# Performance work log

Hardware: AMD Instinct MI355X
Metric: run time of the kernel (lower is better)

Reference implementation:

```python
import jax, jax.numpy as jnp
import numpy as np

CTX_SIZE = 4096
LAYER = 1
N_EMBD = 1024
HEAD_SIZE = 64
B, T = 4, 4096


def setup_inputs() -> dict:
    key = jax.random.key(0)
    ks = jax.random.split(key, 4)
    s = 1.0 / np.sqrt(N_EMBD)
    return {
        "x": jax.random.normal(ks[0], (B, T, N_EMBD), dtype=jnp.float32),
        "Wq": jax.random.normal(ks[1], (N_EMBD, HEAD_SIZE), dtype=jnp.float32) * s,
        "bq": jnp.zeros((HEAD_SIZE,), dtype=jnp.float32),
        "Wk": jax.random.normal(ks[2], (N_EMBD, HEAD_SIZE), dtype=jnp.float32) * s,
        "bk": jnp.zeros((HEAD_SIZE,), dtype=jnp.float32),
        "Wv": jax.random.normal(ks[3], (N_EMBD, HEAD_SIZE), dtype=jnp.float32) * s,
        "bv": jnp.zeros((HEAD_SIZE,), dtype=jnp.float32),
    }


def reference(x, Wq, bq, Wk, bk, Wv, bv):
    Bx, Tx, C = x.shape
    t = CTX_SIZE // (2 ** LAYER)
    cut = min(Tx, t)  # static: shapes are concrete under jit

    k = x @ Wk + bk                      # [B, T, H]
    q = x[:, -cut:, :] @ Wq + bq         # [B, cut, H] (fade: queries on last cut tokens)
    v = x @ Wv + bv                      # [B, T, H]

    att = jnp.einsum("bqh,bkh->bqk", q, k) * (C ** -0.5)  # [B, cut, T]

    # row i corresponds to absolute query position (T - cut + i); causal: key j <= that pos
    q_pos = jnp.arange(cut) + (Tx - cut)   # [cut]
    k_pos = jnp.arange(Tx)                 # [T]
    mask = k_pos[None, :] <= q_pos[:, None]  # [cut, T], True = keep
    att = jnp.where(mask[None, :, :], att, -jnp.inf)
    att = jax.nn.softmax(att, axis=-1)
    # dropout p=0.0 (eval mode): identity

    out = jnp.einsum("bqk,bkh->bqh", att, v)  # [B, cut, H]
    return out
```

## Files before the change

### kernel.cpp

```cpp
#include <hip/hip_runtime.h>

#define BB 4
#define TT 4096
#define CUT 2048
#define CE 1024
#define HD 64
#define QSC 0.045084220027780106f

typedef unsigned short u16;
typedef unsigned int u32;
typedef __attribute__((ext_vector_type(8))) short bf16x8;
typedef __attribute__((ext_vector_type(4))) float f32x4;

__device__ __forceinline__ u16 f2b(float f) {
  union { float f; unsigned u; } v; v.f = f;
  unsigned r = v.u + 0x7fffu + ((v.u >> 16) & 1u);
  return (u16)(r >> 16);
}

__device__ __forceinline__ u32 cvtpk(float lo, float hi) {
  u32 r;
  asm("v_cvt_pk_bf16_f32 %0, %1, %2" : "=v"(r) : "v"(lo), "v"(hi));
  return r;
}

__global__ void wtrans_k(const float* __restrict__ Wk, const float* __restrict__ Wv,
                         const float* __restrict__ Wq, u16* __restrict__ w3f) {
  int id = blockIdx.x * 256 + threadIdx.x;
  int j    = id & 7;
  int lane = (id >> 3) & 63;
  int f    = id >> 9;
  int kstep = f & 31;
  int mnt   = f >> 5;
  int m  = mnt >> 2;
  int nt = mnt & 3;
  int k   = kstep * 32 + (lane >> 4) * 8 + j;
  int col = nt * 16 + (lane & 15);
  const float* W = (m == 0) ? Wk : (m == 1) ? Wv : Wq;
  w3f[id] = f2b(W[k * 64 + col]);
}

__launch_bounds__(256, 2)
__global__ void proj_k(const float* __restrict__ x, const u16* __restrict__ w3f,
                       const float* __restrict__ bk, const float* __restrict__ bv,
                       const float* __restrict__ bq,
                       u16* __restrict__ Kb, u16* __restrict__ Vb, u16* __restrict__ Qb) {
  __shared__ f32x4 cl[2][2][12][64];
  const int tid  = threadIdx.x;
  const int lane = tid & 63;
  const int kh   = tid >> 6;
  const int l15  = lane & 15;
  const int g    = lane >> 4;
  const int r0   = blockIdx.x * 32;

  f32x4 acc[2][12];
  #pragma unroll
  for (int h = 0; h < 2; ++h)
    #pragma unroll
    for (int t = 0; t < 12; ++t) acc[h][t] = (f32x4){0.f, 0.f, 0.f, 0.f};

  const float* x0 = x + (size_t)(r0 + l15) * CE;
  const float* x1 = x + (size_t)(r0 + 16 + l15) * CE;

  #pragma unroll
  for (int kc = 0; kc < 8; ++kc) {
    const int ko = kh * 256 + kc * 32 + g * 8;
    bf16x8 a0, a1;
    {
      f32x4 xa = *(const f32x4*)(x0 + ko);
      f32x4 xb = *(const f32x4*)(x0 + ko + 4);
      f32x4 ya = *(const f32x4*)(x1 + ko);
      f32x4 yb = *(const f32x4*)(x1 + ko + 4);
      #pragma unroll
      for (int j = 0; j < 4; ++j) {
        a0[j] = (short)f2b(xa[j]); a0[j + 4] = (short)f2b(xb[j]);
        a1[j] = (short)f2b(ya[j]); a1[j + 4] = (short)f2b(yb[j]);
      }
    }
    const int kstep = kh * 8 + kc;
    #pragma unroll
    for (int mnt = 0; mnt < 12; ++mnt) {
      bf16x8 bfr = *(const bf16x8*)&w3f[(size_t)(mnt * 32 + kstep) * 512 + lane * 8];
      acc[0][mnt] = __builtin_amdgcn_mfma_f32_16x16x32_bf16(a0, bfr, acc[0][mnt], 0, 0, 0);
      acc[1][mnt] = __builtin_amdgcn_mfma_f32_16x16x32_bf16(a1, bfr, acc[1][mnt], 0, 0, 0);
    }
  }

  if (kh >= 2) {
    #pragma unroll
    for (int h = 0; h < 2; ++h)
      #pragma unroll
      for (int t = 0; t < 12; ++t) cl[kh - 2][h][t][lane] = acc[h][t];
  }
  __syncthreads();
  if (kh < 2) {
    #pragma unroll
    for (int h = 0; h < 2; ++h)
      #pragma unroll
      for (int t = 0; t < 12; ++t) acc[h][t] += cl[kh][h][t][lane];
  }
  __syncthreads();
  if (kh == 1) {
    #pragma unroll
    for (int h = 0; h < 2; ++h)
      #pragma unroll
      for (int t = 0; t < 12; ++t) cl[0][h][t][lane] = acc[h][t];
  }
  __syncthreads();
  if (kh == 0) {
    #pragma unroll
    for (int h = 0; h < 2; ++h)
      #pragma unroll
      for (int t = 0; t < 12; ++t) acc[h][t] += cl[0][h][t][lane];

    #pragma unroll
    for (int h = 0; h < 2; ++h) {
      const int orow0 = r0 + h * 16 + g * 4;
      #pragma unroll
      for (int m = 0; m < 3; ++m) {
        const float* bias = (m == 0) ? bk : (m == 1) ? bv : bq;
        #pragma unroll
        for (int nt = 0; nt < 4; ++nt) {
          int col = nt * 16 + l15;
          float bc = bias[col];
          #pragma unroll
          for (int r = 0; r < 4; ++r) {
            int orow = orow0 + r;
            float val = acc[h][m * 4 + nt][r] + bc;
            if (m == 0)      Kb[(size_t)orow * HD + col] = f2b(val);
            else if (m == 1) Vb[(size_t)orow * HD + col] = f2b(val);
            else {
              int t = orow & (TT - 1);
              if (t >= CUT)
                Qb[((size_t)(orow >> 12) * CUT + (t - CUT)) * HD + col] = f2b(val * QSC);
            }
          }
        }
      }
    }
  }
}

__global__ void kvtrans_k(const u16* __restrict__ Kb, const u16* __restrict__ Vb,
                          u16* __restrict__ KF, u16* __restrict__ VF) {
  int id = blockIdx.x * 256 + threadIdx.x;
  int lane = id & 63;
  int f    = (id >> 6) & 7;
  int c    = (id >> 9) & 63;
  int sel  = id >> 15;
  int l15 = lane & 15, g = lane >> 4;
  if (sel < 4) {
    int b = sel;
    int kt = f >> 1, h = f & 1;
    int row = c * 64 + kt * 16 + l15;
    bf16x8 v = *(const bf16x8*)&Kb[((size_t)b * TT + row) * HD + h * 32 + g * 8];
    *(bf16x8*)&KF[(((size_t)b * 64 + c) * 8 + f) * 512 + lane * 8] = v;
  } else {
    int b = sel - 4;
    int c2 = f >> 2, dt = f & 3;
    int row = c * 64 + c2 * 32 + g * 8;
    int d = dt * 16 + l15;
    const u16* src = Vb + ((size_t)b * TT + row) * HD + d;
    bf16x8 v;
    #pragma unroll
    for (int j = 0; j < 8; ++j) v[j] = (short)src[j * HD];
    *(bf16x8*)&VF[(((size_t)b * 64 + c) * 8 + f) * 512 + lane * 8] = v;
  }
}

__launch_bounds__(512, 4)
__global__ void attn_k(const u16* __restrict__ Qb, const u16* __restrict__ KF,
                       const u16* __restrict__ VF, float* __restrict__ out) {
  __shared__ u32   PLd[8][16][36];
  __shared__ float OO[8][16][66];
  __shared__ float OL[8][16];
  const int tid  = threadIdx.x;
  const int lane = tid & 63;
  const int wv   = tid >> 6;
  const int l15  = lane & 15;
  const int g    = lane >> 4;
  const int id   = blockIdx.x;
  const int b    = id & 3;
  const int i0   = (id >> 2) * 16;

  const int qabs = CUT + i0 + l15;
  const int qmin = CUT + i0;

  const u16* qrow = Qb + ((size_t)b * CUT + i0 + l15) * HD;
  bf16x8 qf0 = *(const bf16x8*)&qrow[g * 8];
  bf16x8 qf1 = *(const bf16x8*)&qrow[32 + g * 8];

  f32x4 o[4];
  #pragma unroll
  for (int dt = 0; dt < 4; ++dt) o[dt] = (f32x4){0.f, 0.f, 0.f, 0.f};
  float lsum = 0.f;

  const int kv_end = CUT + i0 + 16;
  const int nch = (kv_end + 63) >> 6;
  const u16* KFb = KF + (size_t)b * 64 * 8 * 512;
  const u16* VFb = VF + (size_t)b * 64 * 8 * 512;

  for (int c = wv; c < nch; c += 8) {
    const int kv0 = c << 6;

    const u16* kp = KFb + (size_t)c * 4096 + lane * 8;
    bf16x8 ka[4][2];
    #pragma unroll
    for (int kt = 0; kt < 4; ++kt) {
      ka[kt][0] = *(const bf16x8*)(kp + (kt * 2 + 0) * 512);
      ka[kt][1] = *(const bf16x8*)(kp + (kt * 2 + 1) * 512);
    }
    const u16* vp = VFb + (size_t)c * 4096 + lane * 8;
    bf16x8 va[2][4];
    #pragma unroll
    for (int c2 = 0; c2 < 2; ++c2)
      #pragma unroll
      for (int dt = 0; dt < 4; ++dt)
        va[c2][dt] = *(const bf16x8*)(vp + (c2 * 4 + dt) * 512);

    f32x4 st[4];
    __builtin_amdgcn_s_setprio(1);
    #pragma unroll
    for (int kt = 0; kt < 4; ++kt) {
      f32x4 s = (f32x4){0.f, 0.f, 0.f, 0.f};
      s = __builtin_amdgcn_mfma_f32_16x16x32_bf16(ka[kt][0], qf0, s, 0, 0, 0);
      s = __builtin_amdgcn_mfma_f32_16x16x32_bf16(ka[kt][1], qf1, s, 0, 0, 0);
      st[kt] = s;
    }
    __builtin_amdgcn_s_setprio(0);

    if (kv0 + 63 <= qmin) {
      #pragma unroll
      for (int kt = 0; kt < 4; ++kt)
        #pragma unroll
        for (int r = 0; r < 4; ++r) {
          float p = exp2f(st[kt][r]);
          st[kt][r] = p;
          lsum += p;
        }
    } else {
      #pragma unroll
      for (int kt = 0; kt < 4; ++kt)
        #pragma unroll
        for (int r = 0; r < 4; ++r) {
          int key = kv0 + kt * 16 + g * 4 + r;
          float p = exp2f(st[kt][r]);
          p = (key <= qabs) ? p : 0.f;
          st[kt][r] = p;
          lsum += p;
        }
    }

    #pragma unroll
    for (int kt = 0; kt < 4; ++kt) {
      u32 d0 = cvtpk(st[kt][0], st[kt][1]);
      u32 d1 = cvtpk(st[kt][2], st[kt][3]);
      u32* p = &PLd[wv][l15][kt * 8 + g * 2];
      p[0] = d0; p[1] = d1;
    }

    __builtin_amdgcn_s_setprio(1);
    #pragma unroll
    for (int c2 = 0; c2 < 2; ++c2) {
      bf16x8 pa = *(const bf16x8*)&PLd[wv][l15][c2 * 16 + g * 4];
      #pragma unroll
      for (int dt = 0; dt < 4; ++dt)
        o[dt] = __builtin_amdgcn_mfma_f32_16x16x32_bf16(pa, va[c2][dt], o[dt], 0, 0, 0);
    }
    __builtin_amdgcn_s_setprio(0);
  }

  lsum += __shfl_xor(lsum, 16);
  lsum += __shfl_xor(lsum, 32);
  if (lane < 16) OL[wv][l15] = lsum;
  #pragma unroll
  for (int dt = 0; dt < 4; ++dt)
    #pragma unroll
    for (int r = 0; r < 4; ++r)
      OO[wv][g * 4 + r][dt * 16 + l15] = o[dt][r];
  __syncthreads();

  #pragma unroll
  for (int e = tid; e < 1024; e += 512) {
    int q = e >> 6, d = e & 63;
    float L = 0.f, O = 0.f;
    #pragma unroll
    for (int w = 0; w < 8; ++w) { L += OL[w][q]; O += OO[w][q][d]; }
    out[((size_t)b * CUT + i0 + q) * HD + d] = O / L;
  }
}

extern "C" void kernel_launch(void* const* d_in, const int* in_sizes, int n_in,
                              void* d_out, int out_size, void* d_ws, size_t ws_size,
                              hipStream_t stream) {
  const float* x  = (const float*)d_in[0];
  const float* Wq = (const float*)d_in[1];
  const float* bq = (const float*)d_in[2];
  const float* Wk = (const float*)d_in[3];
  const float* bk = (const float*)d_in[4];
  const float* Wv = (const float*)d_in[5];
  const float* bv = (const float*)d_in[6];
  float* out = (float*)d_out;

  u16* Kb  = (u16*)d_ws;
  u16* Vb  = Kb + (size_t)BB * TT * HD;
  u16* Qb  = Vb + (size_t)BB * TT * HD;
  u16* W3F = Qb + (size_t)BB * CUT * HD;
  u16* KF  = W3F + (size_t)384 * 512;
  u16* VF  = KF + (size_t)BB * 64 * 8 * 512;

  wtrans_k<<<768, 256, 0, stream>>>(Wk, Wv, Wq, W3F);
  proj_k<<<512, 256, 0, stream>>>(x, W3F, bk, bv, bq, Kb, Vb, Qb);
  kvtrans_k<<<1024, 256, 0, stream>>>(Kb, Vb, KF, VF);
  attn_k<<<512, 512, 0, stream>>>(Qb, KF, VF, out);
}
```

Before: 58.46 us.

## Fuse K/V fragment transpose into projection epilogue and prefetch x loads

The projection kernel now writes K and V directly in the MFMA fragment layouts the attention kernel consumes, so the separate kvtrans kernel and the intermediate Kb/Vb buffers are removed. The epilogue is split across three waves (Q, K, V) after staging the reduced accumulators in shared memory. It also double-buffers the fp32 x loads one k-chunk ahead so they overlap with the MFMAs. The cost is one extra LDS round trip and sync, scattered 2-byte stores into the fragment layout, and more registers held for the prefetch.

```diff
diff --git a/kernel.cpp b/kernel.cpp
--- a/kernel.cpp
+++ b/kernel.cpp
@@ -44,7 +44,7 @@
 __global__ void proj_k(const float* __restrict__ x, const u16* __restrict__ w3f,
                        const float* __restrict__ bk, const float* __restrict__ bv,
                        const float* __restrict__ bq,
-                       u16* __restrict__ Kb, u16* __restrict__ Vb, u16* __restrict__ Qb) {
+                       u16* __restrict__ KF, u16* __restrict__ VF, u16* __restrict__ Qb) {
   __shared__ f32x4 cl[2][2][12][64];
   const int tid  = threadIdx.x;
   const int lane = tid & 63;
@@ -62,20 +62,30 @@
   const float* x0 = x + (size_t)(r0 + l15) * CE;
   const float* x1 = x + (size_t)(r0 + 16 + l15) * CE;
 
+  f32x4 xs[2][4];
+  {
+    const int ko = kh * 256 + g * 8;
+    xs[0][0] = *(const f32x4*)(x0 + ko);
+    xs[0][1] = *(const f32x4*)(x0 + ko + 4);
+    xs[0][2] = *(const f32x4*)(x1 + ko);
+    xs[0][3] = *(const f32x4*)(x1 + ko + 4);
+  }
+
   #pragma unroll
   for (int kc = 0; kc < 8; ++kc) {
-    const int ko = kh * 256 + kc * 32 + g * 8;
+    const int cur = kc & 1, nxt = cur ^ 1;
+    if (kc < 7) {
+      const int ko = kh * 256 + (kc + 1) * 32 + g * 8;
+      xs[nxt][0] = *(const f32x4*)(x0 + ko);
+      xs[nxt][1] = *(const f32x4*)(x0 + ko + 4);
+      xs[nxt][2] = *(const f32x4*)(x1 + ko);
+      xs[nxt][3] = *(const f32x4*)(x1 + ko + 4);
+    }
     bf16x8 a0, a1;
-    {
-      f32x4 xa = *(const f32x4*)(x0 + ko);
-      f32x4 xb = *(const f32x4*)(x0 + ko + 4);
-      f32x4 ya = *(const f32x4*)(x1 + ko);
-      f32x4 yb = *(const f32x4*)(x1 + ko + 4);
-      #pragma unroll
-      for (int j = 0; j < 4; ++j) {
-        a0[j] = (short)f2b(xa[j]); a0[j + 4] = (short)f2b(xb[j]);
-        a1[j] = (short)f2b(ya[j]); a1[j + 4] = (short)f2b(yb[j]);
-      }
+    #pragma unroll
+    for (int j = 0; j < 4; ++j) {
+      a0[j] = (short)f2b(xs[cur][0][j]); a0[j + 4] = (short)f2b(xs[cur][1][j]);
+      a1[j] = (short)f2b(xs[cur][2][j]); a1[j + 4] = (short)f2b(xs[cur][3][j]);
     }
     const int kstep = kh * 8 + kc;
     #pragma unroll
@@ -112,59 +122,66 @@
     for (int h = 0; h < 2; ++h)
       #pragma unroll
       for (int t = 0; t < 12; ++t) acc[h][t] += cl[0][h][t][lane];
-
-    #pragma unroll
-    for (int h = 0; h < 2; ++h) {
-      const int orow0 = r0 + h * 16 + g * 4;
-      #pragma unroll
-      for (int m = 0; m < 3; ++m) {
-        const float* bias = (m == 0) ? bk : (m == 1) ? bv : bq;
+    #pragma unroll
+    for (int h = 0; h < 2; ++h)
+      #pragma unroll
+      for (int t = 0; t < 8; ++t) cl[1][h][t][lane] = acc[h][t];
+  }
+  __syncthreads();
+
+  const int b    = r0 >> 12;
+  const int cch  = (r0 >> 6) & 63;
+  const int half = (r0 >> 5) & 1;
+
+  if (kh == 0) {
+    const int t0 = r0 & (TT - 1);
+    if (t0 >= CUT) {
+      const int trow = t0 - CUT;
+      #pragma unroll
+      for (int h = 0; h < 2; ++h)
         #pragma unroll
         for (int nt = 0; nt < 4; ++nt) {
           int col = nt * 16 + l15;
-          float bc = bias[col];
+          float bc = bq[col];
           #pragma unroll
           for (int r = 0; r < 4; ++r) {
-            int orow = orow0 + r;
-            float val = acc[h][m * 4 + nt][r] + bc;
-            if (m == 0)      Kb[(size_t)orow * HD + col] = f2b(val);
-            else if (m == 1) Vb[(size_t)orow * HD + col] = f2b(val);
-            else {
-              int t = orow & (TT - 1);
-              if (t >= CUT)
-                Qb[((size_t)(orow >> 12) * CUT + (t - CUT)) * HD + col] = f2b(val * QSC);
-            }
+            int qrow = trow + h * 16 + g * 4 + r;
+            Qb[((size_t)b * CUT + qrow) * HD + col] = f2b((acc[h][8 + nt][r] + bc) * QSC);
           }
         }
+    }
+  } else if (kh == 1) {
+    u16* KFc = KF + ((size_t)(b * 64 + cch) * 8) * 512;
+    #pragma unroll
+    for (int h = 0; h < 2; ++h) {
+      const int kt2 = (half * 2 + h) * 2;
+      #pragma unroll
+      for (int nt = 0; nt < 4; ++nt) {
+        int col = nt * 16 + l15;
+        float bc = bk[col];
+        f32x4 v = cl[1][h][nt][lane];
+        const int off = (kt2 + (nt >> 1)) * 512 + 128 * ((nt & 1) * 2 + (l15 >> 3)) + (l15 & 7);
+        #pragma unroll
+        for (int r = 0; r < 4; ++r)
+          KFc[off + (g * 4 + r) * 8] = f2b(v[r] + bc);
       }
     }
-  }
-}
-
-__global__ void kvtrans_k(const u16* __restrict__ Kb, const u16* __restrict__ Vb,
-                          u16* __restrict__ KF, u16* __restrict__ VF) {
-  int id = blockIdx.x * 256 + threadIdx.x;
-  int lane = id & 63;
-  int f    = (id >> 6) & 7;
-  int c    = (id >> 9) & 63;
-  int sel  = id >> 15;
-  int l15 = lane & 15, g = lane >> 4;
-  if (sel < 4) {
-    int b = sel;
-    int kt = f >> 1, h = f & 1;
-    int row = c * 64 + kt * 16 + l15;
-    bf16x8 v = *(const bf16x8*)&Kb[((size_t)b * TT + row) * HD + h * 32 + g * 8];
-    *(bf16x8*)&KF[(((size_t)b * 64 + c) * 8 + f) * 512 + lane * 8] = v;
-  } else {
-    int b = sel - 4;
-    int c2 = f >> 2, dt = f & 3;
-    int row = c * 64 + c2 * 32 + g * 8;
-    int d = dt * 16 + l15;
-    const u16* src = Vb + ((size_t)b * TT + row) * HD + d;
-    bf16x8 v;
-    #pragma unroll
-    for (int j = 0; j < 8; ++j) v[j] = (short)src[j * HD];
-    *(bf16x8*)&VF[(((size_t)b * 64 + c) * 8 + f) * 512 + lane * 8] = v;
+  } else if (kh == 2) {
+    u16* VFc = VF + ((size_t)(b * 64 + cch) * 8) * 512;
+    #pragma unroll
+    for (int h = 0; h < 2; ++h) {
+      #pragma unroll
+      for (int nt = 0; nt < 4; ++nt) {
+        int col = nt * 16 + l15;
+        float bc = bv[col];
+        f32x4 v = cl[1][h][4 + nt][lane];
+        #pragma unroll
+        for (int r = 0; r < 4; ++r) {
+          int tt = h * 16 + g * 4 + r;
+          VFc[(half * 4 + nt) * 512 + (l15 + 16 * (tt >> 3)) * 8 + (tt & 7)] = f2b(v[r] + bc);
+        }
+      }
+    }
   }
 }
 
@@ -302,15 +319,12 @@
   const float* bv = (const float*)d_in[6];
   float* out = (float*)d_out;
 
-  u16* Kb  = (u16*)d_ws;
-  u16* Vb  = Kb + (size_t)BB * TT * HD;
-  u16* Qb  = Vb + (size_t)BB * TT * HD;
+  u16* Qb  = (u16*)d_ws;
   u16* W3F = Qb + (size_t)BB * CUT * HD;
   u16* KF  = W3F + (size_t)384 * 512;
   u16* VF  = KF + (size_t)BB * 64 * 8 * 512;
 
   wtrans_k<<<768, 256, 0, stream>>>(Wk, Wv, Wq, W3F);
-  proj_k<<<512, 256, 0, stream>>>(x, W3F, bk, bv, bq, Kb, Vb, Qb);
-  kvtrans_k<<<1024, 256, 0, stream>>>(Kb, Vb, KF, VF);
+  proj_k<<<512, 256, 0, stream>>>(x, W3F, bk, bv, bq, KF, VF, Qb);
   attn_k<<<512, 512, 0, stream>>>(Qb, KF, VF, out);
 }
```

Result: faster. 53.41 us (-8.6%).
